# Performance work log

Measured on AMD Instinct MI355X. Metric: run time of the kernel, lower is better.

## Reference

```python
import jax, jax.numpy as jnp
import numpy as np

B, H, NQ, NK, D = 256, 16, 49, 49, 64
SCALE = 1.0 / np.sqrt(D).astype(np.float32)
EPS = 1e-9  # matches kernel's 1/(l + 1e-9)


def setup_inputs() -> dict:
    key = jax.random.key(0)
    kq, kk, kv = jax.random.split(key, 3)
    q = jax.random.normal(kq, (B, H, NQ, D), dtype=jnp.float32)
    k = jax.random.normal(kk, (B, H, NK, D), dtype=jnp.float32)
    v = jax.random.normal(kv, (B, H, NK, D), dtype=jnp.float32)
    return {"q": q, "k": k, "v": v}


def reference(q, k, v):
    # scores: [B,H,Nq,Nk]
    s = jnp.einsum("bhqd,bhkd->bhqk", q, k) * SCALE
    m = jnp.max(s, axis=-1, keepdims=True)
    e = jnp.exp(s - m)
    l = jnp.sum(e, axis=-1, keepdims=True)
    p = e / (l + EPS)  # kernel divides by (l + 1e-9)
    out = jnp.einsum("bhqk,bhkd->bhqd", p, v)
    return out
```

## Files before the change

kernel.cpp:

```cpp
#include <hip/hip_runtime.h>


#define NQA 49
#define DD  64
#define ST  72

typedef __bf16 bf16x4 __attribute__((ext_vector_type(4)));
typedef __bf16 bf16x8 __attribute__((ext_vector_type(8)));
typedef float  f32x4  __attribute__((ext_vector_type(4)));

__device__ __forceinline__ int vt_off(int d, int k) {
    return d * ST + ((((k >> 3) + ((d >> 2) & 7)) & 7) << 3) + (k & 7);
}

__global__ __launch_bounds__(256, 5)
void attn49_kernel(const float* __restrict__ Q, const float* __restrict__ K,
                   const float* __restrict__ V, float* __restrict__ O) {
    __shared__ __bf16 Qs[64 * ST];
    __shared__ __bf16 Ks[64 * ST];
    __shared__ __bf16 Vt[64 * ST];

    const int tid = threadIdx.x;
    const size_t base = (size_t)blockIdx.x * (NQA * DD);
    const float* Qg = Q + base;
    const float* Kg = K + base;
    const float* Vg = V + base;

    {
        const int f  = tid & 15;
        const int r0 = tid >> 4;
        #pragma unroll
        for (int it = 0; it < 4; ++it) {
            const int r = r0 + 16 * it;
            float4 qv = {0.f,0.f,0.f,0.f}, kv = {0.f,0.f,0.f,0.f},
                   vv = {0.f,0.f,0.f,0.f};
            if (r < NQA) {
                qv = *(const float4*)(Qg + r * DD + 4 * f);
                kv = *(const float4*)(Kg + r * DD + 4 * f);
                vv = *(const float4*)(Vg + r * DD + 4 * f);
            }
            bf16x4 qb = { (__bf16)(0.125f*qv.x), (__bf16)(0.125f*qv.y),
                          (__bf16)(0.125f*qv.z), (__bf16)(0.125f*qv.w) };
            bf16x4 kb = { (__bf16)kv.x, (__bf16)kv.y, (__bf16)kv.z, (__bf16)kv.w };
            *(bf16x4*)&Qs[r * ST + 4 * f] = qb;
            *(bf16x4*)&Ks[r * ST + 4 * f] = kb;
            Vt[vt_off(4*f + 0, r)] = (__bf16)vv.x;
            Vt[vt_off(4*f + 1, r)] = (__bf16)vv.y;
            Vt[vt_off(4*f + 2, r)] = (__bf16)vv.z;
            Vt[vt_off(4*f + 3, r)] = (__bf16)vv.w;
        }
    }
    __syncthreads();

    const int w  = tid >> 6;
    const int lr = tid & 15;
    const int lg = (tid >> 4) & 3;

    bf16x8 aq0 = *(const bf16x8*)&Qs[(16*w + lr) * ST      + 8*lg];
    bf16x8 aq1 = *(const bf16x8*)&Qs[(16*w + lr) * ST + 32 + 8*lg];
    f32x4 acc[4] = {};
    #pragma unroll
    for (int t = 0; t < 4; ++t) {
        bf16x8 b0 = *(const bf16x8*)&Ks[(16*t + lr) * ST      + 8*lg];
        bf16x8 b1 = *(const bf16x8*)&Ks[(16*t + lr) * ST + 32 + 8*lg];
        acc[t] = __builtin_amdgcn_mfma_f32_16x16x32_bf16(aq0, b0, acc[t], 0, 0, 0);
        acc[t] = __builtin_amdgcn_mfma_f32_16x16x32_bf16(aq1, b1, acc[t], 0, 0, 0);
    }

    float inv_l[4];
    #pragma unroll
    for (int i = 0; i < 4; ++i) {
        const int gq = 16*w + 4*lg + i;
        float e0 = __expf(acc[0][i]);
        float e1 = __expf(acc[1][i]);
        float e2 = __expf(acc[2][i]);
        float e3 = (lr == 0) ? __expf(acc[3][i]) : 0.f;
        float sum = (e0 + e1) + (e2 + e3);
        #pragma unroll
        for (int d = 1; d < 16; d <<= 1) sum += __shfl_xor(sum, d, 64);
        inv_l[i] = 1.f / (sum + 1e-9f);
        Qs[gq * ST +  0 + lr] = (__bf16)e0;
        Qs[gq * ST + 16 + lr] = (__bf16)e1;
        Qs[gq * ST + 32 + lr] = (__bf16)e2;
        Qs[gq * ST + 48 + lr] = (__bf16)e3;
    }

    bf16x8 ap0 = *(const bf16x8*)&Qs[(16*w + lr) * ST      + 8*lg];
    bf16x8 ap1 = *(const bf16x8*)&Qs[(16*w + lr) * ST + 32 + 8*lg];
    f32x4 oacc[4] = {};
    #pragma unroll
    for (int t = 0; t < 4; ++t) {
        bf16x8 b0 = *(const bf16x8*)&Vt[vt_off(16*t + lr,  8*lg)];
        bf16x8 b1 = *(const bf16x8*)&Vt[vt_off(16*t + lr, 32 + 8*lg)];
        oacc[t] = __builtin_amdgcn_mfma_f32_16x16x32_bf16(ap0, b0, oacc[t], 0, 0, 0);
        oacc[t] = __builtin_amdgcn_mfma_f32_16x16x32_bf16(ap1, b1, oacc[t], 0, 0, 0);
    }

    float* Og = O + base;
    #pragma unroll
    for (int i = 0; i < 4; ++i) {
        const int gq = 16*w + 4*lg + i;
        if (gq < NQA) {
            #pragma unroll
            for (int t = 0; t < 4; ++t)
                Og[gq * DD + 16*t + lr] = oacc[t][i] * inv_l[i];
        }
    }
}

extern "C" void kernel_launch(void* const* d_in, const int* in_sizes, int n_in,
                              void* d_out, int out_size, void* d_ws, size_t ws_size,
                              hipStream_t stream) {
    const float* q = (const float*)d_in[0];
    const float* k = (const float*)d_in[1];
    const float* v = (const float*)d_in[2];
    float* out = (float*)d_out;
    (void)in_sizes; (void)n_in; (void)out_size; (void)d_ws; (void)ws_size;
    attn49_kernel<<<dim3(4096), dim3(256), 0, stream>>>(q, k, v, out);
}
```

Measured before the change: 185.6 us.

## Process four heads per block with register prefetch of next head's inputs

Each block now loops over four heads and issues the global loads for the next head into registers while the current head's MFMA and softmax work runs, aiming to hide global-memory latency. The grid shrinks to a quarter, and the launch-bounds occupancy hint drops from 5 to 4 blocks because of higher register use. The swizzled transposed-V layout is replaced by a plain strided layout, which may add LDS bank conflicts on the V transpose stores and reads.

```diff
diff --git a/kernel.cpp b/kernel.cpp
--- a/kernel.cpp
+++ b/kernel.cpp
@@ -4,16 +4,13 @@
 #define NQA 49
 #define DD  64
 #define ST  72
+#define TT  4
 
 typedef __bf16 bf16x4 __attribute__((ext_vector_type(4)));
 typedef __bf16 bf16x8 __attribute__((ext_vector_type(8)));
 typedef float  f32x4  __attribute__((ext_vector_type(4)));
 
-__device__ __forceinline__ int vt_off(int d, int k) {
-    return d * ST + ((((k >> 3) + ((d >> 2) & 7)) & 7) << 3) + (k & 7);
-}
-
-__global__ __launch_bounds__(256, 5)
+__global__ __launch_bounds__(256, 4)
 void attn49_kernel(const float* __restrict__ Q, const float* __restrict__ K,
                    const float* __restrict__ V, float* __restrict__ O) {
     __shared__ __bf16 Qs[64 * ST];
@@ -21,89 +18,115 @@
     __shared__ __bf16 Vt[64 * ST];
 
     const int tid = threadIdx.x;
-    const size_t base = (size_t)blockIdx.x * (NQA * DD);
-    const float* Qg = Q + base;
-    const float* Kg = K + base;
-    const float* Vg = V + base;
+    const int f  = tid & 15;
+    const int r0 = tid >> 4;
+    const int w  = tid >> 6;
+    const int lr = tid & 15;
+    const int lg = (tid >> 4) & 3;
+    const int head0 = blockIdx.x * TT;
+
+    float4 qv[4], kv[4], vv[4];
 
     {
-        const int f  = tid & 15;
-        const int r0 = tid >> 4;
+        const size_t base = (size_t)head0 * (NQA * DD);
         #pragma unroll
         for (int it = 0; it < 4; ++it) {
             const int r = r0 + 16 * it;
-            float4 qv = {0.f,0.f,0.f,0.f}, kv = {0.f,0.f,0.f,0.f},
-                   vv = {0.f,0.f,0.f,0.f};
+            float4 z = {0.f, 0.f, 0.f, 0.f};
+            qv[it] = z; kv[it] = z; vv[it] = z;
             if (r < NQA) {
-                qv = *(const float4*)(Qg + r * DD + 4 * f);
-                kv = *(const float4*)(Kg + r * DD + 4 * f);
-                vv = *(const float4*)(Vg + r * DD + 4 * f);
+                qv[it] = *(const float4*)(Q + base + r * DD + 4 * f);
+                kv[it] = *(const float4*)(K + base + r * DD + 4 * f);
+                vv[it] = *(const float4*)(V + base + r * DD + 4 * f);
             }
-            bf16x4 qb = { (__bf16)(0.125f*qv.x), (__bf16)(0.125f*qv.y),
-                          (__bf16)(0.125f*qv.z), (__bf16)(0.125f*qv.w) };
-            bf16x4 kb = { (__bf16)kv.x, (__bf16)kv.y, (__bf16)kv.z, (__bf16)kv.w };
+        }
+    }
+
+    #pragma unroll 1
+    for (int t = 0; t < TT; ++t) {
+        __syncthreads();
+
+        #pragma unroll
+        for (int it = 0; it < 4; ++it) {
+            const int r = r0 + 16 * it;
+            bf16x4 qb = { (__bf16)(0.125f * qv[it].x), (__bf16)(0.125f * qv[it].y),
+                          (__bf16)(0.125f * qv[it].z), (__bf16)(0.125f * qv[it].w) };
+            bf16x4 kb = { (__bf16)kv[it].x, (__bf16)kv[it].y,
+                          (__bf16)kv[it].z, (__bf16)kv[it].w };
             *(bf16x4*)&Qs[r * ST + 4 * f] = qb;
             *(bf16x4*)&Ks[r * ST + 4 * f] = kb;
-            Vt[vt_off(4*f + 0, r)] = (__bf16)vv.x;
-            Vt[vt_off(4*f + 1, r)] = (__bf16)vv.y;
-            Vt[vt_off(4*f + 2, r)] = (__bf16)vv.z;
-            Vt[vt_off(4*f + 3, r)] = (__bf16)vv.w;
+            Vt[(4*f + 0) * ST + r] = (__bf16)vv[it].x;
+            Vt[(4*f + 1) * ST + r] = (__bf16)vv[it].y;
+            Vt[(4*f + 2) * ST + r] = (__bf16)vv[it].z;
+            Vt[(4*f + 3) * ST + r] = (__bf16)vv[it].w;
         }
-    }
-    __syncthreads();
 
-    const int w  = tid >> 6;
-    const int lr = tid & 15;
-    const int lg = (tid >> 4) & 3;
+        if (t + 1 < TT) {
+            const size_t base = (size_t)(head0 + t + 1) * (NQA * DD);
+            #pragma unroll
+            for (int it = 0; it < 4; ++it) {
+                const int r = r0 + 16 * it;
+                float4 z = {0.f, 0.f, 0.f, 0.f};
+                qv[it] = z; kv[it] = z; vv[it] = z;
+                if (r < NQA) {
+                    qv[it] = *(const float4*)(Q + base + r * DD + 4 * f);
+                    kv[it] = *(const float4*)(K + base + r * DD + 4 * f);
+                    vv[it] = *(const float4*)(V + base + r * DD + 4 * f);
+                }
+            }
+        }
 
-    bf16x8 aq0 = *(const bf16x8*)&Qs[(16*w + lr) * ST      + 8*lg];
-    bf16x8 aq1 = *(const bf16x8*)&Qs[(16*w + lr) * ST + 32 + 8*lg];
-    f32x4 acc[4] = {};
-    #pragma unroll
-    for (int t = 0; t < 4; ++t) {
-        bf16x8 b0 = *(const bf16x8*)&Ks[(16*t + lr) * ST      + 8*lg];
-        bf16x8 b1 = *(const bf16x8*)&Ks[(16*t + lr) * ST + 32 + 8*lg];
-        acc[t] = __builtin_amdgcn_mfma_f32_16x16x32_bf16(aq0, b0, acc[t], 0, 0, 0);
-        acc[t] = __builtin_amdgcn_mfma_f32_16x16x32_bf16(aq1, b1, acc[t], 0, 0, 0);
-    }
+        __syncthreads();
 
-    float inv_l[4];
-    #pragma unroll
-    for (int i = 0; i < 4; ++i) {
-        const int gq = 16*w + 4*lg + i;
-        float e0 = __expf(acc[0][i]);
-        float e1 = __expf(acc[1][i]);
-        float e2 = __expf(acc[2][i]);
-        float e3 = (lr == 0) ? __expf(acc[3][i]) : 0.f;
-        float sum = (e0 + e1) + (e2 + e3);
+        bf16x8 aq0 = *(const bf16x8*)&Qs[(16*w + lr) * ST      + 8*lg];
+        bf16x8 aq1 = *(const bf16x8*)&Qs[(16*w + lr) * ST + 32 + 8*lg];
+        f32x4 acc[4] = {};
         #pragma unroll
-        for (int d = 1; d < 16; d <<= 1) sum += __shfl_xor(sum, d, 64);
-        inv_l[i] = 1.f / (sum + 1e-9f);
-        Qs[gq * ST +  0 + lr] = (__bf16)e0;
-        Qs[gq * ST + 16 + lr] = (__bf16)e1;
-        Qs[gq * ST + 32 + lr] = (__bf16)e2;
-        Qs[gq * ST + 48 + lr] = (__bf16)e3;
-    }
+        for (int tt = 0; tt < 4; ++tt) {
+            bf16x8 b0 = *(const bf16x8*)&Ks[(16*tt + lr) * ST      + 8*lg];
+            bf16x8 b1 = *(const bf16x8*)&Ks[(16*tt + lr) * ST + 32 + 8*lg];
+            acc[tt] = __builtin_amdgcn_mfma_f32_16x16x32_bf16(aq0, b0, acc[tt], 0, 0, 0);
+            acc[tt] = __builtin_amdgcn_mfma_f32_16x16x32_bf16(aq1, b1, acc[tt], 0, 0, 0);
+        }
 
-    bf16x8 ap0 = *(const bf16x8*)&Qs[(16*w + lr) * ST      + 8*lg];
-    bf16x8 ap1 = *(const bf16x8*)&Qs[(16*w + lr) * ST + 32 + 8*lg];
-    f32x4 oacc[4] = {};
-    #pragma unroll
-    for (int t = 0; t < 4; ++t) {
-        bf16x8 b0 = *(const bf16x8*)&Vt[vt_off(16*t + lr,  8*lg)];
-        bf16x8 b1 = *(const bf16x8*)&Vt[vt_off(16*t + lr, 32 + 8*lg)];
-        oacc[t] = __builtin_amdgcn_mfma_f32_16x16x32_bf16(ap0, b0, oacc[t], 0, 0, 0);
-        oacc[t] = __builtin_amdgcn_mfma_f32_16x16x32_bf16(ap1, b1, oacc[t], 0, 0, 0);
-    }
+        float inv_l[4];
+        #pragma unroll
+        for (int i = 0; i < 4; ++i) {
+            const int gq = 16*w + 4*lg + i;
+            float e0 = __expf(acc[0][i]);
+            float e1 = __expf(acc[1][i]);
+            float e2 = __expf(acc[2][i]);
+            float e3 = (lr == 0) ? __expf(acc[3][i]) : 0.f;
+            float sum = (e0 + e1) + (e2 + e3);
+            #pragma unroll
+            for (int d = 1; d < 16; d <<= 1) sum += __shfl_xor(sum, d, 64);
+            inv_l[i] = 1.f / (sum + 1e-9f);
+            Qs[gq * ST +  0 + lr] = (__bf16)e0;
+            Qs[gq * ST + 16 + lr] = (__bf16)e1;
+            Qs[gq * ST + 32 + lr] = (__bf16)e2;
+            Qs[gq * ST + 48 + lr] = (__bf16)e3;
+        }
 
-    float* Og = O + base;
-    #pragma unroll
-    for (int i = 0; i < 4; ++i) {
-        const int gq = 16*w + 4*lg + i;
-        if (gq < NQA) {
-            #pragma unroll
-            for (int t = 0; t < 4; ++t)
-                Og[gq * DD + 16*t + lr] = oacc[t][i] * inv_l[i];
+        bf16x8 ap0 = *(const bf16x8*)&Qs[(16*w + lr) * ST      + 8*lg];
+        bf16x8 ap1 = *(const bf16x8*)&Qs[(16*w + lr) * ST + 32 + 8*lg];
+        f32x4 oacc[4] = {};
+        #pragma unroll
+        for (int tt = 0; tt < 4; ++tt) {
+            bf16x8 b0 = *(const bf16x8*)&Vt[(16*tt + lr) * ST      + 8*lg];
+            bf16x8 b1 = *(const bf16x8*)&Vt[(16*tt + lr) * ST + 32 + 8*lg];
+            oacc[tt] = __builtin_amdgcn_mfma_f32_16x16x32_bf16(ap0, b0, oacc[tt], 0, 0, 0);
+            oacc[tt] = __builtin_amdgcn_mfma_f32_16x16x32_bf16(ap1, b1, oacc[tt], 0, 0, 0);
+        }
+
+        float* Og = O + (size_t)(head0 + t) * (NQA * DD);
+        #pragma unroll
+        for (int i = 0; i < 4; ++i) {
+            const int gq = 16*w + 4*lg + i;
+            if (gq < NQA) {
+                #pragma unroll
+                for (int tt = 0; tt < 4; ++tt)
+                    Og[gq * DD + 16*tt + lr] = oacc[tt][i] * inv_l[i];
+            }
         }
     }
 }
@@ -116,5 +139,5 @@
     const float* v = (const float*)d_in[2];
     float* out = (float*)d_out;
     (void)in_sizes; (void)n_in; (void)out_size; (void)d_ws; (void)ws_size;
-    attn49_kernel<<<dim3(4096), dim3(256), 0, stream>>>(q, k, v, out);
+    attn49_kernel<<<dim3(4096 / TT), dim3(256), 0, stream>>>(q, k, v, out);
 }
```

Result: slower. 191.3 us (+3.1%).
